# Optimization experiments

Hardware: AMD Instinct MI355X
Metric: run time of the kernel (lower is better)

Reference implementation:

```python
import jax, jax.numpy as jnp
import numpy as np

V, E, H, B, S = 32000, 512, 1024, 32, 64
NL = 1
EOS = 1


def setup_inputs() -> dict:
    key = jax.random.key(0)
    ks = jax.random.split(key, 16)
    w = lambda k, shp: jax.random.normal(k, shp, jnp.float32) * 0.05
    return dict(
        targets=jax.random.randint(ks[0], (B, S), 0, V),
        targets_kws=jax.random.randint(ks[1], (B, S), 0, V),
        sent_state=jax.random.normal(ks[2], (NL, B, H), jnp.float32),
        targets_len=jax.random.randint(ks[3], (B,), 0, S),
        emb_W=w(ks[4], (V, E)),
        w_Wih=w(ks[5], (3 * H, 2 * E)), w_Whh=w(ks[6], (3 * H, H)),
        w_bih=w(ks[7], (3 * H,)), w_bhh=w(ks[8], (3 * H,)),
        s_Wih=w(ks[9], (3 * H, H)), s_Whh=w(ks[10], (3 * H, H)),
        s_bih=w(ks[11], (3 * H,)), s_bhh=w(ks[12], (3 * H,)),
        out_W=w(ks[13], (V, H)), out_b=w(ks[14], (V,)),
    )


def _gru_step(x, h, Wih, Whh, bih, bhh):
    # PyTorch GRU cell math (gate order r, z, n)
    gi = x @ Wih.T + bih          # [B, 3H]
    gh = h @ Whh.T + bhh          # [B, 3H]
    ir, iz, inn = jnp.split(gi, 3, axis=1)
    hr, hz, hn = jnp.split(gh, 3, axis=1)
    r = jax.nn.sigmoid(ir + hr)
    z = jax.nn.sigmoid(iz + hz)
    n = jnp.tanh(inn + r * hn)
    return (1.0 - z) * n + z * h


def reference(targets, targets_kws, sent_state, targets_len,
              emb_W, w_Wih, w_Whh, w_bih, w_bhh,
              s_Wih, s_Whh, s_bih, s_bhh, out_W, out_b):
    # per-step index sequences, time-major [S-1, B]
    lw = targets[:, :-1].T        # last word at step i
    kw = targets_kws[:, 1:].T     # keyword i+1
    nxt = targets[:, 1:].T        # prediction target i+1
    steps = jnp.arange(1, targets.shape[1])  # i+1 values for len mask

    def step(carry, inp):
        word_h, sent_h, loss = carry
        lw_t, kw_t, nxt_t, t = inp
        x = jnp.concatenate([emb_W[kw_t], emb_W[lw_t]], axis=1)  # [B, 2E]
        wh = _gru_step(x, word_h, w_Wih, w_Whh, w_bih, w_bhh)    # word_output == word_state (nl=1)
        logp = jax.nn.log_softmax(wh @ out_W.T + out_b, axis=-1)  # [B, V]
        tmp = _gru_step(wh, sent_h, s_Wih, s_Whh, s_bih, s_bhh)
        m = (nxt_t == EOS).astype(wh.dtype)[:, None]              # EOS blend mask [B,1]
        new_sent = sent_h * (1.0 - m) + tmp * m
        new_word = wh * (1.0 - m) + tmp * m
        g = jnp.take_along_axis(logp, nxt_t[:, None], axis=1)[:, 0]
        valid = (targets_len > t).astype(wh.dtype)
        return (new_word, new_sent, loss + jnp.sum(g * valid)), None

    word0 = sent_state[0]
    sent0 = sent_state[0]
    (_, _, loss), _ = jax.lax.scan(step, (word0, sent0, jnp.float32(0.0)),
                                   (lw, kw, nxt, steps))
    return -loss
```

## Files before the change

### kernel.cpp

```cpp
#include <hip/hip_runtime.h>

typedef __attribute__((ext_vector_type(8))) short short8;
typedef __attribute__((ext_vector_type(4))) float float4v;
typedef __attribute__((ext_vector_type(4))) unsigned short ushort4v;

#define DEV __device__ __forceinline__
#define AGENT __HIP_MEMORY_SCOPE_AGENT

DEV unsigned short f2bf(float f) {
  union { float f; unsigned u; } v; v.f = f;
  unsigned r = v.u + 0x7fffu + ((v.u >> 16) & 1u);
  return (unsigned short)(r >> 16);
}
DEV float bf2f(unsigned short h) {
  union { unsigned u; float f; } v; v.u = ((unsigned)h) << 16;
  return v.f;
}

DEV void gl2lds16(const void* g, void* l) {
  __builtin_amdgcn_global_load_lds(
      (const __attribute__((address_space(1))) void*)g,
      (__attribute__((address_space(3))) void*)l, 16, 0, 0);
}

DEV void ast32(unsigned short* p, unsigned v) {
  __hip_atomic_store((unsigned*)p, v, __ATOMIC_RELAXED, AGENT);
}
DEV short8 ald16(const unsigned short* p) {
  unsigned long long lo = __hip_atomic_load((const unsigned long long*)p,     __ATOMIC_RELAXED, AGENT);
  unsigned long long hi = __hip_atomic_load((const unsigned long long*)p + 1, __ATOMIC_RELAXED, AGENT);
  union { unsigned long long q[2]; short8 s; } u;
  u.q[0] = lo; u.q[1] = hi;
  return u.s;
}

DEV void bar(unsigned* flags, unsigned epoch) {
  __syncthreads();
  if (threadIdx.x < 64) {
    const int lane = threadIdx.x;
    if (lane == 0)
      __hip_atomic_store(&flags[blockIdx.x * 32], epoch, __ATOMIC_RELAXED, AGENT);
    bool ok = false;
    do {
      ok = ok || (__hip_atomic_load(&flags[lane * 32], __ATOMIC_RELAXED, AGENT) >= epoch);
    } while (!__all(ok));
  }
  __syncthreads();
}

__global__ __launch_bounds__(256) void zero_flags(unsigned* p, int n) {
  int i = blockIdx.x * 256 + threadIdx.x;
  if (i < n) p[i] = 0;
}

__global__ __launch_bounds__(256) void cvt4(const float* __restrict__ in,
                                            unsigned short* __restrict__ out, int n4) {
  const int idx = blockIdx.x * 256 + threadIdx.x;
  if (idx >= n4) return;
  float4 v = ((const float4*)in)[idx];
  ushort4v o = { f2bf(v.x), f2bf(v.y), f2bf(v.z), f2bf(v.w) };
  ((ushort4v*)out)[idx] = o;
}

__global__ __launch_bounds__(256) void gatherx(const float* __restrict__ emb,
                                               const int* __restrict__ targets,
                                               const int* __restrict__ tkws,
                                               unsigned short* __restrict__ X) {
  const int row = blockIdx.x;
  const int i = row >> 5, b = row & 31;
  const int t = threadIdx.x;
  const int kw = tkws[b * 64 + i + 1];
  const int lw = targets[b * 64 + i];
  const float4* src = (t < 128) ? (const float4*)(emb + (size_t)kw * 512)
                                : (const float4*)(emb + (size_t)lw * 512);
  const int c = t & 127;
  float4 v = src[c];
  ushort4v o = { f2bf(v.x), f2bf(v.y), f2bf(v.z), f2bf(v.w) };
  ((ushort4v*)(X + (size_t)row * 1024))[(t < 128 ? 0 : 128) + c] = o;
}

__global__ __launch_bounds__(256, 1) void gemm_bt0(
    const unsigned short* __restrict__ A,
    const unsigned short* __restrict__ B,
    float* __restrict__ out,
    int ldc) {
  __shared__ __align__(16) unsigned short As[128 * 32];
  __shared__ __align__(16) unsigned short Bs[128 * 32];
  const int tid = threadIdx.x;
  const int w = tid >> 6, lane = tid & 63;
  const int r4 = lane >> 2, c4 = lane & 3;
  const int m0 = blockIdx.x * 128, n0 = blockIdx.y * 128;
  const int m_off = (w & 1) * 64, n_off = (w >> 1) * 64;
  const int lrow = lane & 15, lk = (lane >> 4) * 8;

  const unsigned short* Ab = A + (size_t)(m0 + w * 16 + r4) * 1024 + c4 * 8;
  const unsigned short* Bb = B + (size_t)(n0 + w * 16 + r4) * 1024 + c4 * 8;

  float4v acc[4][4] = {};

  for (int k0 = 0; k0 < 1024; k0 += 32) {
    gl2lds16(Ab + k0,             &As[w * 512]);
    gl2lds16(Ab + 64 * 1024 + k0, &As[2048 + w * 512]);
    gl2lds16(Bb + k0,             &Bs[w * 512]);
    gl2lds16(Bb + 64 * 1024 + k0, &Bs[2048 + w * 512]);
    __syncthreads();
    short8 af[4], bfr[4];
#pragma unroll
    for (int t = 0; t < 4; t++) {
      af[t]  = *(const short8*)&As[(m_off + t * 16 + lrow) * 32 + lk];
      bfr[t] = *(const short8*)&Bs[(n_off + t * 16 + lrow) * 32 + lk];
    }
#pragma unroll
    for (int mt = 0; mt < 4; mt++)
#pragma unroll
      for (int nt = 0; nt < 4; nt++)
        acc[mt][nt] = __builtin_amdgcn_mfma_f32_16x16x32_bf16(af[mt], bfr[nt], acc[mt][nt], 0, 0, 0);
    __syncthreads();
  }

#pragma unroll
  for (int mt = 0; mt < 4; mt++) {
    const int gr = m0 + m_off + mt * 16 + (lane >> 4) * 4;
#pragma unroll
    for (int nt = 0; nt < 4; nt++) {
      const int gc = n0 + n_off + nt * 16 + lrow;
#pragma unroll
      for (int rg = 0; rg < 4; rg++)
        out[(size_t)(gr + rg) * ldc + gc] = acc[mt][nt][rg];
    }
  }
}

__global__ __launch_bounds__(256, 1) void fused_kernel(
    const float* __restrict__ Gi,
    const unsigned short* __restrict__ WhhB,
    const unsigned short* __restrict__ sWihB,
    const unsigned short* __restrict__ sWhhB,
    unsigned short* __restrict__ h_bf,
    unsigned short* __restrict__ sent_bf,
    unsigned short* __restrict__ WH,
    const float* __restrict__ w_bih, const float* __restrict__ w_bhh,
    const float* __restrict__ s_bih, const float* __restrict__ s_bhh,
    const int* __restrict__ targets,
    const float* __restrict__ sent_state,
    unsigned* __restrict__ flags,
    unsigned* __restrict__ gflags,
    const float* __restrict__ outW,
    unsigned short* __restrict__ outWb,
    float* __restrict__ parts,
    const float* __restrict__ out_b) {
  __shared__ __align__(16) unsigned char smem[117248];
  const int tid = threadIdx.x;
  const int lane = tid & 63, wv = tid >> 6;

  unsigned long long eosmask;
  {
    bool e = false;
    if (lane < 63)
      for (int b = 0; b < 32; b++) e |= (targets[b * 64 + lane + 1] == 1);
    eosmask = __ballot(e);
  }

  if (blockIdx.x >= 64) {
    const int wg = blockIdx.x - 64;
    unsigned short* As = (unsigned short*)smem;
    unsigned short* Bs = (unsigned short*)(smem + 8192);
    float*          msb = (float*)(smem + 16384);

    for (int idx = wg * 256 + tid; idx < 8192000; idx += 192 * 256) {
      float4 v = ((const float4*)outW)[idx];
      unsigned p0 = (unsigned)f2bf(v.x) | ((unsigned)f2bf(v.y) << 16);
      unsigned p1 = (unsigned)f2bf(v.z) | ((unsigned)f2bf(v.w) << 16);
      unsigned long long pq = (unsigned long long)p0 | ((unsigned long long)p1 << 32);
      __hip_atomic_store((unsigned long long*)&outWb[(size_t)idx * 4], pq,
                         __ATOMIC_RELAXED, AGENT);
    }
    __syncthreads();
    if (tid == 0)
      __hip_atomic_store(&gflags[wg * 32], 1u, __ATOMIC_RELAXED, AGENT);
    if (tid < 64) {
      bool o0 = false, o1 = false, o2 = false;
      while (true) {
        o0 = o0 || (__hip_atomic_load(&gflags[tid * 32],         __ATOMIC_RELAXED, AGENT) != 0u);
        o1 = o1 || (__hip_atomic_load(&gflags[(64 + tid) * 32],  __ATOMIC_RELAXED, AGENT) != 0u);
        o2 = o2 || (__hip_atomic_load(&gflags[(128 + tid) * 32], __ATOMIC_RELAXED, AGENT) != 0u);
        if (__all(o0 && o1 && o2)) break;
        __builtin_amdgcn_s_sleep(32);
      }
    }
    __syncthreads();

    const int w = wv;
    const int r4 = lane >> 2, c4 = lane & 3;
    const int lrow = lane & 15, lk = (lane >> 4) * 8;
    const int m_off = (w & 1) * 64, n_off = (w >> 1) * 64;
    int gated_mt = -1;
    for (int bi = wg; bi < 4000; bi += 192) {
      const int mt = bi / 250, nt = bi - mt * 250;
      if (mt > gated_mt) {
        const int L = (4 * mt + 3 > 62) ? 62 : (4 * mt + 3);
        const unsigned E = 2u + (unsigned)L +
            (unsigned)__popcll(eosmask & ((1ull << L) - 1ull));
        if (tid < 64) {
          bool ok = false;
          while (true) {
            ok = ok || (__hip_atomic_load(&flags[tid * 32], __ATOMIC_RELAXED, AGENT) >= E);
            if (__all(ok)) break;
            __builtin_amdgcn_s_sleep(32);
          }
        }
        __syncthreads();
        gated_mt = mt;
      }
      const int m0 = mt * 128, n0 = nt * 128;
      const unsigned short* Ab = WH    + (size_t)(m0 + w * 16 + r4) * 1024 + c4 * 8;
      const unsigned short* Bb = outWb + (size_t)(n0 + w * 16 + r4) * 1024 + c4 * 8;
      float4v acc[4][4] = {};
      for (int k0 = 0; k0 < 1024; k0 += 32) {
        gl2lds16(Ab + k0,             &As[w * 512]);
        gl2lds16(Ab + 64 * 1024 + k0, &As[2048 + w * 512]);
        gl2lds16(Bb + k0,             &Bs[w * 512]);
        gl2lds16(Bb + 64 * 1024 + k0, &Bs[2048 + w * 512]);
        __syncthreads();
        short8 af[4], bfr[4];
#pragma unroll
        for (int t = 0; t < 4; t++) {
          af[t]  = *(const short8*)&As[(m_off + t * 16 + lrow) * 32 + lk];
          bfr[t] = *(const short8*)&Bs[(n_off + t * 16 + lrow) * 32 + lk];
        }
#pragma unroll
        for (int a = 0; a < 4; a++)
#pragma unroll
          for (int b = 0; b < 4; b++)
            acc[a][b] = __builtin_amdgcn_mfma_f32_16x16x32_bf16(af[a], bfr[b], acc[a][b], 0, 0, 0);
        __syncthreads();
      }
      float b4[4];
#pragma unroll
      for (int b = 0; b < 4; b++) b4[b] = out_b[n0 + n_off + b * 16 + lrow];
#pragma unroll
      for (int a = 0; a < 4; a++) {
#pragma unroll
        for (int rg = 0; rg < 4; rg++) {
          float v0 = acc[a][0][rg] + b4[0];
          float v1 = acc[a][1][rg] + b4[1];
          float v2 = acc[a][2][rg] + b4[2];
          float v3 = acc[a][3][rg] + b4[3];
          float mx = fmaxf(fmaxf(v0, v1), fmaxf(v2, v3));
#pragma unroll
          for (int d = 1; d < 16; d <<= 1) mx = fmaxf(mx, __shfl_xor(mx, d, 64));
          float s = __expf(v0 - mx) + __expf(v1 - mx) + __expf(v2 - mx) + __expf(v3 - mx);
#pragma unroll
          for (int d = 1; d < 16; d <<= 1) s += __shfl_xor(s, d, 64);
          if ((lane & 15) == 0) {
            int r = m_off + a * 16 + (lane >> 4) * 4 + rg;
            msb[(w >> 1) * 256 + r * 2 + 0] = mx;
            msb[(w >> 1) * 256 + r * 2 + 1] = s;
          }
        }
      }
      __syncthreads();
      if (tid < 128) {
        float m1 = msb[tid * 2], s1 = msb[tid * 2 + 1];
        float m2 = msb[256 + tid * 2], s2 = msb[256 + tid * 2 + 1];
        float M = fmaxf(m1, m2);
        float S = s1 * __expf(m1 - M) + s2 * __expf(m2 - M);
        ((float2*)parts)[(size_t)(m0 + tid) * 250 + nt] = make_float2(M, S);
      }
      __syncthreads();
    }
    return;
  }

  unsigned short* WhhS = (unsigned short*)smem;
  float (*Cred)[32][49] = (float (*)[32][49])(smem + 98304);
  float (*hsl)[16] = (float (*)[16])(smem + 110848);
  float (*ssl)[16] = (float (*)[16])(smem + 112896);
  float (*whsl)[16] = (float (*)[16])(smem + 114944);

  const int khalf = wv >> 1, mtile = wv & 1;
  const int jb = blockIdx.x * 16;
  const int lr = lane & 15;
  const int bb = mtile * 16 + lr;
  const int kb = khalf * 512 + (lane >> 4) * 8;
  const int cb = kb >> 3;
  const int swz = lr & 7;
  const int b0 = (tid * 2) >> 4, j0 = (tid * 2) & 15;
  unsigned epoch = 0;
  int scur = 0;

  for (int idx = tid; idx < 6144; idx += 256) {
    const int R = idx >> 7, c = idx & 127;
    const int g = R >> 4, rr = R & 15;
    short8 v = *(const short8*)&WhhB[((size_t)(g * 1024 + jb + rr)) * 1024 + c * 8];
    *(short8*)&WhhS[(R * 128 + (c ^ (rr & 7))) * 8] = v;
  }

  float bi[2][3], bh[2][3];
#pragma unroll
  for (int u = 0; u < 2; u++)
#pragma unroll
    for (int g = 0; g < 3; g++) {
      bi[u][g] = w_bih[g * 1024 + jb + j0 + u];
      bh[u][g] = w_bhh[g * 1024 + jb + j0 + u];
    }

  {
    float v0 = sent_state[b0 * 1024 + jb + j0];
    float v1 = sent_state[b0 * 1024 + jb + j0 + 1];
    hsl[b0][j0] = v0; hsl[b0][j0 + 1] = v1;
    ssl[b0][j0] = v0; ssl[b0][j0 + 1] = v1;
    unsigned pv = (unsigned)f2bf(v0) | ((unsigned)f2bf(v1) << 16);
    ast32(&h_bf[b0 * 1024 + jb + j0], pv);
    ast32(&sent_bf[b0 * 1024 + jb + j0], pv);
  }

  float2 gp[3];
  {
    const float* p = Gi + (size_t)b0 * 3072 + jb + j0;
    gp[0] = *(const float2*)(p);
    gp[1] = *(const float2*)(p + 1024);
    gp[2] = *(const float2*)(p + 2048);
  }

  epoch++; bar(flags, epoch);

  for (int i = 0; i < 63; i++) {
    const unsigned short* hr = h_bf + (i & 1) * 32768;
    unsigned short*       hw = h_bf + ((i + 1) & 1) * 32768;
    const bool anyeos = (eosmask >> i) & 1;

    short8 a[16];
#pragma unroll
    for (int ks = 0; ks < 16; ks++)
      a[ks] = ald16(&hr[bb * 1024 + kb + ks * 32]);
    float4v acc[3] = {};
#pragma unroll
    for (int ks = 0; ks < 16; ks++) {
#pragma unroll
      for (int g = 0; g < 3; g++) {
        short8 b8 = *(const short8*)&WhhS[((g * 16 + lr) * 128 + ((cb + ks * 4) ^ swz)) * 8];
        acc[g] = __builtin_amdgcn_mfma_f32_16x16x32_bf16(a[ks], b8, acc[g], 0, 0, 0);
      }
    }
#pragma unroll
    for (int g = 0; g < 3; g++)
#pragma unroll
      for (int rg = 0; rg < 4; rg++)
        Cred[khalf][mtile * 16 + (lane >> 4) * 4 + rg][g * 16 + lr] = acc[g][rg];
    __syncthreads();

    float wh2[2];
#pragma unroll
    for (int u = 0; u < 2; u++) {
      const int jj = j0 + u;
      float ghr = Cred[0][b0][jj]      + Cred[1][b0][jj]      + bh[u][0];
      float ghz = Cred[0][b0][16 + jj] + Cred[1][b0][16 + jj] + bh[u][1];
      float ghn = Cred[0][b0][32 + jj] + Cred[1][b0][32 + jj] + bh[u][2];
      float gir = ((float*)&gp[0])[u] + bi[u][0];
      float giz = ((float*)&gp[1])[u] + bi[u][1];
      float gin = ((float*)&gp[2])[u] + bi[u][2];
      float r = 1.f / (1.f + __expf(-(gir + ghr)));
      float z = 1.f / (1.f + __expf(-(giz + ghz)));
      float n = tanhf(gin + r * ghn);
      float wh = (1.f - z) * n + z * hsl[b0][jj];
      whsl[b0][jj] = wh;
      wh2[u] = wh;
    }
    {
      unsigned pv = (unsigned)f2bf(wh2[0]) | ((unsigned)f2bf(wh2[1]) << 16);
      ast32(&WH[(size_t)(i * 32 + b0) * 1024 + jb + j0], pv);
    }

    if (i < 62) {
      const float* p = Gi + (size_t)((i + 1) * 32 + b0) * 3072 + jb + j0;
      gp[0] = *(const float2*)(p);
      gp[1] = *(const float2*)(p + 1024);
      gp[2] = *(const float2*)(p + 2048);
    }

    if (!anyeos) {
      hsl[b0][j0] = wh2[0]; hsl[b0][j0 + 1] = wh2[1];
      unsigned pv = (unsigned)f2bf(wh2[0]) | ((unsigned)f2bf(wh2[1]) << 16);
      ast32(&hw[b0 * 1024 + jb + j0], pv);
      epoch++; bar(flags, epoch);
    } else {
      epoch++; bar(flags, epoch);
      const unsigned short* sr = sent_bf + scur * 32768;
      unsigned short*       sw = sent_bf + (scur ^ 1) * 32768;
      short8 a2[16];
#pragma unroll
      for (int ks = 0; ks < 16; ks++)
        a2[ks] = ald16(&WH[(size_t)(i * 32 + bb) * 1024 + kb + ks * 32]);
      float4v acc2[3] = {};
#pragma unroll
      for (int ks = 0; ks < 16; ks++) {
#pragma unroll
        for (int g = 0; g < 3; g++) {
          short8 b8 = *(const short8*)&sWihB[(size_t)(g * 1024 + jb + lr) * 1024 + kb + ks * 32];
          acc2[g] = __builtin_amdgcn_mfma_f32_16x16x32_bf16(a2[ks], b8, acc2[g], 0, 0, 0);
        }
      }
#pragma unroll
      for (int g = 0; g < 3; g++)
#pragma unroll
        for (int rg = 0; rg < 4; rg++)
          Cred[khalf][mtile * 16 + (lane >> 4) * 4 + rg][g * 16 + lr] = acc2[g][rg];
      __syncthreads();
      float gis[2][3];
#pragma unroll
      for (int u = 0; u < 2; u++) {
        const int jj = j0 + u;
#pragma unroll
        for (int g = 0; g < 3; g++)
          gis[u][g] = Cred[0][b0][g * 16 + jj] + Cred[1][b0][g * 16 + jj] + s_bih[g * 1024 + jb + jj];
      }
      __syncthreads();
      short8 a3[16];
#pragma unroll
      for (int ks = 0; ks < 16; ks++)
        a3[ks] = ald16(&sr[bb * 1024 + kb + ks * 32]);
      float4v acc3[3] = {};
#pragma unroll
      for (int ks = 0; ks < 16; ks++) {
#pragma unroll
        for (int g = 0; g < 3; g++) {
          short8 b8 = *(const short8*)&sWhhB[(size_t)(g * 1024 + jb + lr) * 1024 + kb + ks * 32];
          acc3[g] = __builtin_amdgcn_mfma_f32_16x16x32_bf16(a3[ks], b8, acc3[g], 0, 0, 0);
        }
      }
#pragma unroll
      for (int g = 0; g < 3; g++)
#pragma unroll
        for (int rg = 0; rg < 4; rg++)
          Cred[khalf][mtile * 16 + (lane >> 4) * 4 + rg][g * 16 + lr] = acc3[g][rg];
      __syncthreads();
      float ns2[2], nw2[2];
#pragma unroll
      for (int u = 0; u < 2; u++) {
        const int jj = j0 + u;
        float shr = Cred[0][b0][jj]      + Cred[1][b0][jj]      + s_bhh[jb + jj];
        float shz = Cred[0][b0][16 + jj] + Cred[1][b0][16 + jj] + s_bhh[1024 + jb + jj];
        float shn = Cred[0][b0][32 + jj] + Cred[1][b0][32 + jj] + s_bhh[2048 + jb + jj];
        float r = 1.f / (1.f + __expf(-(gis[u][0] + shr)));
        float z = 1.f / (1.f + __expf(-(gis[u][1] + shz)));
        float n = tanhf(gis[u][2] + r * shn);
        float s_old = ssl[b0][jj];
        float tmp = (1.f - z) * n + z * s_old;
        bool m = (targets[b0 * 64 + i + 1] == 1);
        ns2[u] = m ? tmp : s_old;
        nw2[u] = m ? tmp : whsl[b0][jj];
        ssl[b0][jj] = ns2[u];
        hsl[b0][jj] = nw2[u];
      }
      unsigned pvs = (unsigned)f2bf(ns2[0]) | ((unsigned)f2bf(ns2[1]) << 16);
      unsigned pvh = (unsigned)f2bf(nw2[0]) | ((unsigned)f2bf(nw2[1]) << 16);
      ast32(&sw[b0 * 1024 + jb + j0], pvs);
      ast32(&hw[b0 * 1024 + jb + j0], pvh);
      scur ^= 1;
      epoch++; bar(flags, epoch);
    }
  }
}

__global__ __launch_bounds__(256) void row_loss(
    const unsigned short* __restrict__ WH,
    const unsigned short* __restrict__ outWb,
    const float* __restrict__ out_b,
    const int* __restrict__ targets,
    const int* __restrict__ targets_len,
    const float2* __restrict__ partials,
    float* __restrict__ term) {
  const int wv = threadIdx.x >> 6, lane = threadIdx.x & 63;
  const int row = blockIdx.x * 4 + wv;
  const int b = row & 31, i = row >> 5;
  const int tgt = targets[b * 64 + i + 1];
  const short8* a8 = (const short8*)(WH + (size_t)row * 1024);
  const short8* w8 = (const short8*)(outWb + (size_t)tgt * 1024);
  float s = 0.f;
#pragma unroll
  for (int c = 0; c < 2; c++) {
    short8 av = a8[lane + 64 * c];
    short8 wv8 = w8[lane + 64 * c];
#pragma unroll
    for (int j = 0; j < 8; j++)
      s += bf2f((unsigned short)av[j]) * bf2f((unsigned short)wv8[j]);
  }
#pragma unroll
  for (int d = 32; d; d >>= 1) s += __shfl_xor(s, d, 64);

  float m = -1e30f, ssum = 0.f;
  for (int vt = lane; vt < 250; vt += 64) {
    float2 pp = partials[(size_t)row * 250 + vt];
    float nm = fmaxf(m, pp.x);
    ssum = ssum * __expf(m - nm) + pp.y * __expf(pp.x - nm);
    m = nm;
  }
#pragma unroll
  for (int d = 32; d; d >>= 1) {
    float om = __shfl_xor(m, d, 64);
    float os = __shfl_xor(ssum, d, 64);
    float nm = fmaxf(m, om);
    ssum = ssum * __expf(m - nm) + os * __expf(om - nm);
    m = nm;
  }
  if (lane == 0) {
    float y = s + out_b[tgt];
    float lse = m + logf(ssum);
    float valid = (targets_len[b] > i + 1) ? 1.f : 0.f;
    term[row] = valid * (y - lse);
  }
}

__global__ void final_sum(const float* __restrict__ term, float* __restrict__ out) {
  __shared__ float red[256];
  float s = 0.f;
  for (int r = threadIdx.x; r < 2016; r += 256) s += term[r];
  red[threadIdx.x] = s;
  __syncthreads();
  for (int st = 128; st; st >>= 1) {
    if ((int)threadIdx.x < st) red[threadIdx.x] += red[threadIdx.x + st];
    __syncthreads();
  }
  if (threadIdx.x == 0) out[0] = -red[0];
}

extern "C" void kernel_launch(void* const* d_in, const int* in_sizes, int n_in,
                              void* d_out, int out_size, void* d_ws, size_t ws_size,
                              hipStream_t stream) {
  const int*   targets     = (const int*)d_in[0];
  const int*   targets_kws = (const int*)d_in[1];
  const float* sent_state  = (const float*)d_in[2];
  const int*   targets_len = (const int*)d_in[3];
  const float* emb_W       = (const float*)d_in[4];
  const float* w_Wih       = (const float*)d_in[5];
  const float* w_Whh       = (const float*)d_in[6];
  const float* w_bih       = (const float*)d_in[7];
  const float* w_bhh       = (const float*)d_in[8];
  const float* s_Wih       = (const float*)d_in[9];
  const float* s_Whh       = (const float*)d_in[10];
  const float* s_bih       = (const float*)d_in[11];
  const float* s_bhh       = (const float*)d_in[12];
  const float* out_W       = (const float*)d_in[13];
  const float* out_b       = (const float*)d_in[14];

  char* base = (char*)d_ws;
  size_t off = 0;
  auto alloc = [&](size_t bytes) -> void* {
    void* r = base + off;
    off += (bytes + 255) & ~(size_t)255;
    return r;
  };
  unsigned short* outWb   = (unsigned short*)alloc(32000ull * 1024 * 2);
  unsigned short* WihB    = (unsigned short*)alloc(3072ull * 1024 * 2);
  unsigned short* WhhB    = (unsigned short*)alloc(3072ull * 1024 * 2);
  unsigned short* sWihB   = (unsigned short*)alloc(3072ull * 1024 * 2);
  unsigned short* sWhhB   = (unsigned short*)alloc(3072ull * 1024 * 2);
  unsigned short* Xb      = (unsigned short*)alloc(2048ull * 1024 * 2);
  float*          Gi      = (float*)alloc(2048ull * 3072 * 4);
  unsigned short* WH      = (unsigned short*)alloc(2048ull * 1024 * 2);
  unsigned short* h_bf    = (unsigned short*)alloc(2 * 32ull * 1024 * 2);
  unsigned short* sent_bf = (unsigned short*)alloc(2 * 32ull * 1024 * 2);
  float2*         parts   = (float2*)alloc(2048ull * 250 * 8);
  float*          term    = (float*)alloc(2048ull * 4);
  unsigned*       flags   = (unsigned*)alloc(8192 * 4);
  unsigned*       gflags  = flags + 2048;

  zero_flags<<<32, 256, 0, stream>>>(flags, 8192);
  cvt4<<<3072, 256, 0, stream>>>(w_Wih, WihB, 786432);
  cvt4<<<3072, 256, 0, stream>>>(w_Whh, WhhB, 786432);
  cvt4<<<3072, 256, 0, stream>>>(s_Wih, sWihB, 786432);
  cvt4<<<3072, 256, 0, stream>>>(s_Whh, sWhhB, 786432);
  gatherx<<<2016, 256, 0, stream>>>(emb_W, targets, targets_kws, Xb);
  gemm_bt0<<<dim3(16, 24), 256, 0, stream>>>(Xb, WihB, Gi, 3072);

  fused_kernel<<<dim3(256), dim3(256), 0, stream>>>(
      Gi, WhhB, sWihB, sWhhB, h_bf, sent_bf, WH,
      w_bih, w_bhh, s_bih, s_bhh, targets, sent_state,
      flags, gflags, out_W, outWb, (float*)parts, out_b);

  row_loss<<<504, 256, 0, stream>>>(WH, outWb, out_b, targets, targets_len, parts, term);
  final_sum<<<1, 256, 0, stream>>>(term, (float*)d_out);
}
```

Measured before the change: 878.4 us.

## Widen vocab GEMM tile to 128x256 and double-buffer LDS staging

The output-projection GEMM tile inside the fused kernel grows from 128x128 to 128x256 along the vocabulary, so each wave holds a 4x8 accumulator block and each block reuses its A tile across twice as many columns. K-loop staging now ping-pongs between two LDS buffers, issuing the next slice's global-to-LDS loads before the current slice's MFMAs, with one barrier per iteration instead of two. The partial max/sum buffer and the row_loss reduction shrink from 250 to 125 vocab tiles. The cost is more accumulator registers, which may lower occupancy or cause spills, and fewer tiles (2000 over 192 workgroups), which worsens load balance.

Result: faster. 772.4 us (-12.1%).

```diff
diff --git a/kernel.cpp b/kernel.cpp
--- a/kernel.cpp
+++ b/kernel.cpp
@@ -163,9 +163,9 @@
 
   if (blockIdx.x >= 64) {
     const int wg = blockIdx.x - 64;
-    unsigned short* As = (unsigned short*)smem;
-    unsigned short* Bs = (unsigned short*)(smem + 8192);
-    float*          msb = (float*)(smem + 16384);
+    unsigned short* As0 = (unsigned short*)smem;
+    unsigned short* Bs0 = (unsigned short*)(smem + 16384);
+    float*          msb = (float*)(smem + 49152);
 
     for (int idx = wg * 256 + tid; idx < 8192000; idx += 192 * 256) {
       float4 v = ((const float4*)outW)[idx];
@@ -193,10 +193,10 @@
     const int w = wv;
     const int r4 = lane >> 2, c4 = lane & 3;
     const int lrow = lane & 15, lk = (lane >> 4) * 8;
-    const int m_off = (w & 1) * 64, n_off = (w >> 1) * 64;
+    const int m_off = (w & 1) * 64, n_off = (w >> 1) * 128;
     int gated_mt = -1;
-    for (int bi = wg; bi < 4000; bi += 192) {
-      const int mt = bi / 250, nt = bi - mt * 250;
+    for (int bi = wg; bi < 2000; bi += 192) {
+      const int mt = bi / 125, nt = bi - mt * 125;
       if (mt > gated_mt) {
         const int L = (4 * mt + 3 > 62) ? 62 : (4 * mt + 3);
         const unsigned E = 2u + (unsigned)L +
@@ -212,44 +212,65 @@
         __syncthreads();
         gated_mt = mt;
       }
-      const int m0 = mt * 128, n0 = nt * 128;
+      const int m0 = mt * 128, n0 = nt * 256;
       const unsigned short* Ab = WH    + (size_t)(m0 + w * 16 + r4) * 1024 + c4 * 8;
       const unsigned short* Bb = outWb + (size_t)(n0 + w * 16 + r4) * 1024 + c4 * 8;
-      float4v acc[4][4] = {};
-      for (int k0 = 0; k0 < 1024; k0 += 32) {
-        gl2lds16(Ab + k0,             &As[w * 512]);
-        gl2lds16(Ab + 64 * 1024 + k0, &As[2048 + w * 512]);
-        gl2lds16(Bb + k0,             &Bs[w * 512]);
-        gl2lds16(Bb + 64 * 1024 + k0, &Bs[2048 + w * 512]);
-        __syncthreads();
-        short8 af[4], bfr[4];
-#pragma unroll
-        for (int t = 0; t < 4; t++) {
-          af[t]  = *(const short8*)&As[(m_off + t * 16 + lrow) * 32 + lk];
-          bfr[t] = *(const short8*)&Bs[(n_off + t * 16 + lrow) * 32 + lk];
-        }
+      float4v acc[4][8] = {};
+
+#define STAGE(buf, k0)                                                        \
+      {                                                                       \
+        unsigned short* A_ = As0 + (buf) * 4096;                              \
+        unsigned short* B_ = Bs0 + (buf) * 8192;                              \
+        gl2lds16(Ab + (k0),              A_ + (w * 16) * 32);                 \
+        gl2lds16(Ab + 64 * 1024 + (k0),  A_ + (64 + w * 16) * 32);            \
+        gl2lds16(Bb + (k0),              B_ + (w * 16) * 32);                 \
+        gl2lds16(Bb + 64 * 1024 + (k0),  B_ + (64 + w * 16) * 32);            \
+        gl2lds16(Bb + 128 * 1024 + (k0), B_ + (128 + w * 16) * 32);           \
+        gl2lds16(Bb + 192 * 1024 + (k0), B_ + (192 + w * 16) * 32);           \
+      }
+
+      int cur = 0;
+      STAGE(0, 0)
+      __syncthreads();
+      for (int t = 0; t < 32; ++t) {
+        if (t < 31) STAGE(cur ^ 1, (t + 1) * 32)
+        const unsigned short* A_ = As0 + cur * 4096;
+        const unsigned short* B_ = Bs0 + cur * 8192;
+        short8 af[4], bfr[8];
+#pragma unroll
+        for (int x = 0; x < 4; x++)
+          af[x] = *(const short8*)&A_[(m_off + x * 16 + lrow) * 32 + lk];
+#pragma unroll
+        for (int y = 0; y < 8; y++)
+          bfr[y] = *(const short8*)&B_[(n_off + y * 16 + lrow) * 32 + lk];
 #pragma unroll
         for (int a = 0; a < 4; a++)
 #pragma unroll
-          for (int b = 0; b < 4; b++)
+          for (int b = 0; b < 8; b++)
             acc[a][b] = __builtin_amdgcn_mfma_f32_16x16x32_bf16(af[a], bfr[b], acc[a][b], 0, 0, 0);
         __syncthreads();
-      }
-      float b4[4];
-#pragma unroll
-      for (int b = 0; b < 4; b++) b4[b] = out_b[n0 + n_off + b * 16 + lrow];
+        cur ^= 1;
+      }
+#undef STAGE
+
+      float b8v[8];
+#pragma unroll
+      for (int b = 0; b < 8; b++) b8v[b] = out_b[n0 + n_off + b * 16 + lrow];
 #pragma unroll
       for (int a = 0; a < 4; a++) {
 #pragma unroll
         for (int rg = 0; rg < 4; rg++) {
-          float v0 = acc[a][0][rg] + b4[0];
-          float v1 = acc[a][1][rg] + b4[1];
-          float v2 = acc[a][2][rg] + b4[2];
-          float v3 = acc[a][3][rg] + b4[3];
-          float mx = fmaxf(fmaxf(v0, v1), fmaxf(v2, v3));
+          float vv[8];
+#pragma unroll
+          for (int b = 0; b < 8; b++) vv[b] = acc[a][b][rg] + b8v[b];
+          float mx = vv[0];
+#pragma unroll
+          for (int b = 1; b < 8; b++) mx = fmaxf(mx, vv[b]);
 #pragma unroll
           for (int d = 1; d < 16; d <<= 1) mx = fmaxf(mx, __shfl_xor(mx, d, 64));
-          float s = __expf(v0 - mx) + __expf(v1 - mx) + __expf(v2 - mx) + __expf(v3 - mx);
+          float s = 0.f;
+#pragma unroll
+          for (int b = 0; b < 8; b++) s += __expf(vv[b] - mx);
 #pragma unroll
           for (int d = 1; d < 16; d <<= 1) s += __shfl_xor(s, d, 64);
           if ((lane & 15) == 0) {
@@ -265,7 +286,7 @@
         float m2 = msb[256 + tid * 2], s2 = msb[256 + tid * 2 + 1];
         float M = fmaxf(m1, m2);
         float S = s1 * __expf(m1 - M) + s2 * __expf(m2 - M);
-        ((float2*)parts)[(size_t)(m0 + tid) * 250 + nt] = make_float2(M, S);
+        ((float2*)parts)[(size_t)(m0 + tid) * 125 + nt] = make_float2(M, S);
       }
       __syncthreads();
     }
@@ -490,8 +511,8 @@
   for (int d = 32; d; d >>= 1) s += __shfl_xor(s, d, 64);
 
   float m = -1e30f, ssum = 0.f;
-  for (int vt = lane; vt < 250; vt += 64) {
-    float2 pp = partials[(size_t)row * 250 + vt];
+  for (int vt = lane; vt < 125; vt += 64) {
+    float2 pp = partials[(size_t)row * 125 + vt];
     float nm = fmaxf(m, pp.x);
     ssum = ssum * __expf(m - nm) + pp.y * __expf(pp.x - nm);
     m = nm;
@@ -561,7 +582,7 @@
   unsigned short* WH      = (unsigned short*)alloc(2048ull * 1024 * 2);
   unsigned short* h_bf    = (unsigned short*)alloc(2 * 32ull * 1024 * 2);
   unsigned short* sent_bf = (unsigned short*)alloc(2 * 32ull * 1024 * 2);
-  float2*         parts   = (float2*)alloc(2048ull * 250 * 8);
+  float2*         parts   = (float2*)alloc(2048ull * 125 * 8);
   float*          term    = (float*)alloc(2048ull * 4);
   unsigned*       flags   = (unsigned*)alloc(8192 * 4);
   unsigned*       gflags  = flags + 2048;
```
